# Kernel optimization log

Hardware: AMD Instinct MI355X
Metric: run time of the kernel (lower is better)

Reference implementation:

```python
import jax, jax.numpy as jnp
import numpy as np

N_NODES = 100000
N_EDGES = 500000
HEADS = 4
HID = 64
N_GRAPHS = 512
EPS_SM = 1e-8
EPS_BN = 1e-5


def setup_inputs() -> dict:
    key = jax.random.key(0)
    ks = jax.random.split(key, 8)
    x = jax.random.normal(ks[0], (N_NODES, HID), dtype=jnp.float32)
    edge_index = jax.random.randint(ks[1], (2, N_EDGES), 0, N_NODES, dtype=jnp.int64)
    batch = jnp.sort(jax.random.randint(ks[2], (N_NODES,), 0, N_GRAPHS, dtype=jnp.int64))
    Ws = jax.random.normal(ks[3], (3, HEADS * HID, HID), dtype=jnp.float32) * 0.08
    att_src = jax.random.normal(ks[4], (3, HEADS, HID), dtype=jnp.float32) * 0.1
    att_dst = jax.random.normal(ks[5], (3, HEADS, HID), dtype=jnp.float32) * 0.1
    bn_gamma = jnp.ones((2, HID), dtype=jnp.float32)
    bn_beta = jnp.zeros((2, HID), dtype=jnp.float32)
    bn_mean = jnp.zeros((2, HID), dtype=jnp.float32)
    bn_var = jnp.ones((2, HID), dtype=jnp.float32)
    fc_w = jax.random.normal(ks[6], (2, HID), dtype=jnp.float32) * 0.1
    fc_b = jnp.zeros((2,), dtype=jnp.float32)
    return {"x": x, "edge_index": edge_index, "batch": batch, "Ws": Ws,
            "att_src": att_src, "att_dst": att_dst, "bn_gamma": bn_gamma,
            "bn_beta": bn_beta, "bn_mean": bn_mean, "bn_var": bn_var,
            "fc_w": fc_w, "fc_b": fc_b}


def gat_layer(x, row, col, W, a_src, a_dst):
    # x: [N, F] -> h: [N, H, C]
    n = x.shape[0]
    h = (x @ W.T).reshape(n, HEADS, HID)
    a_s = jnp.sum(h * a_src[None], axis=-1)          # [N, H]
    a_d = jnp.sum(h * a_dst[None], axis=-1)          # [N, H]
    e = a_s[row] + a_d[col]                          # [E, H]
    e = jnp.where(e >= 0, e, 0.2 * e)                # LeakyReLU(0.2)
    # segment softmax over destination node (col)
    e_max = jax.ops.segment_max(e, col, num_segments=n)  # [N, H]
    p = jnp.exp(e - e_max[col])
    p_sum = jax.ops.segment_sum(p, col, num_segments=n)
    alpha = p / (p_sum[col] + EPS_SM)                # [E, H]
    msg = h[row] * alpha[:, :, None]                 # [E, H, C]
    out = jax.ops.segment_sum(msg, col, num_segments=n)  # [N, H, C]
    return out.mean(axis=1)                          # [N, C]


def reference(x, edge_index, batch, Ws, att_src, att_dst,
              bn_gamma, bn_beta, bn_mean, bn_var, fc_w, fc_b):
    row, col = edge_index[0], edge_index[1]
    h = x
    for i in range(2):  # first num_layers-1 layers: conv -> BN(eval) -> ReLU
        h = gat_layer(h, row, col, Ws[i], att_src[i], att_dst[i])
        h = (h - bn_mean[i]) * jax.lax.rsqrt(bn_var[i] + EPS_BN) * bn_gamma[i] + bn_beta[i]
        h = jax.nn.relu(h)
        # dropout is inactive in eval mode
    h = gat_layer(h, row, col, Ws[2], att_src[2], att_dst[2])
    # global mean pool over graphs in batch
    sums = jax.ops.segment_sum(h, batch, num_segments=N_GRAPHS)          # [G, C]
    cnts = jax.ops.segment_sum(jnp.ones_like(batch, dtype=h.dtype), batch,
                               num_segments=N_GRAPHS)                    # [G]
    pooled = sums / jnp.maximum(cnts, 1.0)[:, None]
    return pooled @ fc_w.T + fc_b                                        # [G, out]
```

## Files before the change

### kernel.cpp

```cpp
#include <hip/hip_runtime.h>


#define THREADS 256
#define LDP 36
#define SFP 68

__global__ __launch_bounds__(THREADS) void k_prep(
    const float* __restrict__ Ws, const float* __restrict__ att_src,
    const float* __restrict__ att_dst, float* __restrict__ fold)
{
    int idx = blockIdx.x * THREADS + threadIdx.x;
    if (idx >= 3 * 2 * 4 * 64) return;
    int k = idx & 63, head = (idx >> 6) & 3, sd = (idx >> 8) & 1, l = idx >> 9;
    const float* att = (sd ? att_dst : att_src) + l * 256 + head * 64;
    const float* Wb  = Ws + (size_t)l * 16384 + (size_t)head * 64 * 64;
    float s = 0.f;
    #pragma unroll
    for (int c = 0; c < 64; ++c) s = fmaf(Wb[(size_t)c * 64 + k], att[c], s);
    fold[((l * 2 + sd) * 4 + head) * 64 + k] = s;
}

__global__ __launch_bounds__(THREADS) void k_gemm(
    const float* __restrict__ x, const float* __restrict__ W,
    const float* __restrict__ fold_l,
    float* __restrict__ h, float* __restrict__ a_s, float* __restrict__ a_d, int n)
{
    __shared__ float xs[128][LDP];
    __shared__ float ws[128][LDP];
    __shared__ float sf[8 * SFP];
    const int tid  = threadIdx.x;
    const int tc   = tid & 15;
    const int tr   = tid >> 4;
    const int row0 = blockIdx.x * 128;
    const int col0 = blockIdx.y * 128;
    const bool gy0 = (blockIdx.y == 0);

    if (gy0) {
        #pragma unroll
        for (int j = 0; j < 2; ++j) {
            int idx = j * 256 + tid;
            sf[(idx >> 6) * SFP + (idx & 63)] = fold_l[idx];
        }
    }

    float acc[8][8];
    #pragma unroll
    for (int i = 0; i < 8; ++i)
        #pragma unroll
        for (int j = 0; j < 8; ++j) acc[i][j] = 0.f;
    float pa[4] = {0.f, 0.f, 0.f, 0.f};

    for (int ks2 = 0; ks2 < 2; ++ks2) {
        #pragma unroll
        for (int i = 0; i < 4; ++i) {
            int flat4 = i * 256 + tid;
            int r  = flat4 >> 3;
            int c4 = flat4 & 7;
            int gr = row0 + r;
            float4 v = make_float4(0.f, 0.f, 0.f, 0.f);
            if (gr < n) v = *(const float4*)(x + (size_t)gr * 64 + ks2 * 32 + c4 * 4);
            *(float4*)&xs[r][c4 * 4] = v;
            int gp = col0 + r;
            int pr = (gp & 3) * 64 + (gp >> 2);
            float4 wv = *(const float4*)(W + (size_t)pr * 64 + ks2 * 32 + c4 * 4);
            *(float4*)&ws[r][c4 * 4] = wv;
        }
        __syncthreads();

        #pragma unroll 1
        for (int ks = 0; ks < 8; ++ks) {
            float4 xr[8];
            #pragma unroll
            for (int i = 0; i < 8; ++i) xr[i] = *(const float4*)&xs[tr + 16 * i][ks * 4];
            #pragma unroll
            for (int j = 0; j < 8; ++j) {
                float4 w4 = *(const float4*)&ws[tc + 16 * j][ks * 4];
                #pragma unroll
                for (int i = 0; i < 8; ++i) {
                    acc[i][j] = fmaf(xr[i].x, w4.x, acc[i][j]);
                    acc[i][j] = fmaf(xr[i].y, w4.y, acc[i][j]);
                    acc[i][j] = fmaf(xr[i].z, w4.z, acc[i][j]);
                    acc[i][j] = fmaf(xr[i].w, w4.w, acc[i][j]);
                }
            }
        }
        if (gy0) {
            const int vec = tid & 7;
            #pragma unroll
            for (int j = 0; j < 4; ++j) {
                int row = j * 32 + (tid >> 3);
                float s = 0.f;
                #pragma unroll
                for (int k = 0; k < 32; ++k)
                    s = fmaf(xs[row][k], sf[vec * SFP + ks2 * 32 + k], s);
                pa[j] += s;
            }
        }
        __syncthreads();
    }

    #pragma unroll
    for (int i = 0; i < 8; ++i) {
        int r = row0 + tr + 16 * i;
        if (r < n) {
            float* hp = h + (size_t)r * 256 + col0 + tc;
            #pragma unroll
            for (int j = 0; j < 8; ++j) hp[16 * j] = acc[i][j];
        }
    }
    if (gy0) {
        const int vec = tid & 7;
        #pragma unroll
        for (int j = 0; j < 4; ++j) {
            int rr = row0 + j * 32 + (tid >> 3);
            if (rr < n) {
                if (vec < 4) a_s[(size_t)rr * 4 + vec] = pa[j];
                else         a_d[(size_t)rr * 4 + (vec - 4)] = pa[j];
            }
        }
    }
}

__global__ __launch_bounds__(THREADS) void k_hist(
    const int* __restrict__ col, int* __restrict__ hist, int E)
{
    int e = blockIdx.x * THREADS + threadIdx.x;
    if (e < E) atomicAdd(hist + col[e], 1);
}

__global__ __launch_bounds__(THREADS) void k_scan1(
    const int* __restrict__ hist, int* __restrict__ offs, int* __restrict__ partials, int n)
{
    __shared__ int buf0[256], buf1[256];
    int tid = threadIdx.x;
    int i = blockIdx.x * 256 + tid;
    int v = (i < n) ? hist[i] : 0;
    buf0[tid] = v;
    __syncthreads();
    int* src = buf0; int* dst = buf1;
    #pragma unroll
    for (int off = 1; off < 256; off <<= 1) {
        int t = src[tid];
        if (tid >= off) t += src[tid - off];
        dst[tid] = t;
        __syncthreads();
        int* tmp = src; src = dst; dst = tmp;
    }
    if (i < n) offs[i] = src[tid] - v;
    if (tid == 255) partials[blockIdx.x] = src[255];
}

__global__ __launch_bounds__(512) void k_scan2(int* __restrict__ partials, int nb)
{
    __shared__ int buf0[512], buf1[512];
    int tid = threadIdx.x;
    int v = (tid < nb) ? partials[tid] : 0;
    buf0[tid] = v;
    __syncthreads();
    int* src = buf0; int* dst = buf1;
    #pragma unroll
    for (int off = 1; off < 512; off <<= 1) {
        int t = src[tid];
        if (tid >= off) t += src[tid - off];
        dst[tid] = t;
        __syncthreads();
        int* tmp = src; src = dst; dst = tmp;
    }
    if (tid < nb) partials[tid] = src[tid] - v;
}

__global__ __launch_bounds__(THREADS) void k_scan3(
    int* __restrict__ offs, const int* __restrict__ partials, int n)
{
    int i = blockIdx.x * THREADS + threadIdx.x;
    if (i < n) offs[i] += partials[i >> 8];
}

__global__ __launch_bounds__(THREADS) void k_scatter(
    const int* __restrict__ row, const int* __restrict__ col,
    const int* __restrict__ offs, int* __restrict__ tmpc,
    int* __restrict__ rs, int* __restrict__ pose, int E)
{
    int e = blockIdx.x * THREADS + threadIdx.x;
    if (e >= E) return;
    int c = col[e];
    int pos = offs[c] + atomicAdd(tmpc + c, 1);
    rs[pos] = row[e];
    pose[e] = pos;
}

__global__ __launch_bounds__(THREADS) void k_score_ns(
    const int* __restrict__ row, const int* __restrict__ col,
    const int* __restrict__ pose,
    const float* __restrict__ a_s, const float* __restrict__ a_d,
    float* __restrict__ alpha, int E)
{
    int e = blockIdx.x * THREADS + threadIdx.x;
    if (e >= E) return;
    int r = row[e], c = col[e];
    float4 as = *(const float4*)(a_s + (size_t)r * 4);
    float4 ad = *(const float4*)(a_d + (size_t)c * 4);
    float v0 = as.x + ad.x, v1 = as.y + ad.y, v2 = as.z + ad.z, v3 = as.w + ad.w;
    v0 = v0 >= 0.f ? v0 : 0.2f * v0;
    v1 = v1 >= 0.f ? v1 : 0.2f * v1;
    v2 = v2 >= 0.f ? v2 : 0.2f * v2;
    v3 = v3 >= 0.f ? v3 : 0.2f * v3;
    *(float4*)(alpha + (size_t)pose[e] * 4) = make_float4(v0, v1, v2, v3);
}

__global__ __launch_bounds__(THREADS) void k_alpha2(
    const int* __restrict__ offs, const int* __restrict__ deg,
    float* __restrict__ alpha, float* __restrict__ psum, int n)
{
    int v = blockIdx.x * THREADS + threadIdx.x;
    if (v >= n) return;
    const int start = offs[v];
    const int d     = deg[v];
    float m0 = -1e30f, m1 = -1e30f, m2 = -1e30f, m3 = -1e30f;
    for (int i = 0; i < d; ++i) {
        float4 s = *(const float4*)(alpha + (size_t)(start + i) * 4);
        m0 = fmaxf(m0, s.x); m1 = fmaxf(m1, s.y);
        m2 = fmaxf(m2, s.z); m3 = fmaxf(m3, s.w);
    }
    float ps0 = 0.f, ps1 = 0.f, ps2 = 0.f, ps3 = 0.f;
    for (int i = 0; i < d; ++i) {
        float4 s = *(const float4*)(alpha + (size_t)(start + i) * 4);
        float p0 = __expf(s.x - m0), p1 = __expf(s.y - m1);
        float p2 = __expf(s.z - m2), p3 = __expf(s.w - m3);
        ps0 += p0; ps1 += p1; ps2 += p2; ps3 += p3;
        *(float4*)(alpha + (size_t)(start + i) * 4) = make_float4(p0, p1, p2, p3);
    }
    *(float4*)(psum + (size_t)v * 4) = make_float4(ps0, ps1, ps2, ps3);
}

__global__ __launch_bounds__(THREADS) void k_gat(
    const int* __restrict__ rs, const int* __restrict__ offs, const int* __restrict__ deg,
    const float* __restrict__ alpha, const float* __restrict__ psum,
    const float* __restrict__ h,
    const float* __restrict__ bng, const float* __restrict__ bnb,
    const float* __restrict__ bnm, const float* __restrict__ bnv, int use_bn,
    float* __restrict__ out, int n)
{
    int wid  = (blockIdx.x * THREADS + threadIdx.x) >> 6;
    int lane = threadIdx.x & 63;
    if (wid >= n) return;
    const int start = offs[wid];
    const int d     = deg[wid];
    float4 ps = *(const float4*)(psum + (size_t)wid * 4);
    const float i0 = 0.25f / (ps.x + 1e-8f), i1 = 0.25f / (ps.y + 1e-8f);
    const float i2 = 0.25f / (ps.z + 1e-8f), i3 = 0.25f / (ps.w + 1e-8f);

    float acc = 0.f;
    for (int i = 0; i < d; ++i) {
        int r = rs[start + i];
        float4 a = *(const float4*)(alpha + (size_t)(start + i) * 4);
        float4 v = *(const float4*)(h + (size_t)r * 256 + lane * 4);
        acc = fmaf(a.x * i0, v.x, acc);
        acc = fmaf(a.y * i1, v.y, acc);
        acc = fmaf(a.z * i2, v.z, acc);
        acc = fmaf(a.w * i3, v.w, acc);
    }
    if (use_bn) {
        float scale = bng[lane] * rsqrtf(bnv[lane] + 1e-5f);
        float shift = bnb[lane] - bnm[lane] * scale;
        acc = fmaxf(fmaf(acc, scale, shift), 0.f);
    }
    out[(size_t)wid * 64 + lane] = acc;
}

#define POOL_CHUNK 32
__global__ __launch_bounds__(THREADS) void k_pool(
    const float* __restrict__ xf, const int* __restrict__ batch,
    float* __restrict__ sums, float* __restrict__ cnt, int n)
{
    int wid  = (blockIdx.x * THREADS + threadIdx.x) >> 6;
    int lane = threadIdx.x & 63;
    int n0 = wid * POOL_CHUNK;
    if (n0 >= n) return;
    int n1 = min(n0 + POOL_CHUNK, n);
    int g = batch[n0];
    float acc = 0.f, c = 0.f;
    for (int i = n0; i < n1; ++i) {
        int gi = batch[i];
        if (gi != g) {
            atomicAdd(sums + (size_t)g * 64 + lane, acc);
            if (lane == 0) atomicAdd(cnt + g, c);
            g = gi; acc = 0.f; c = 0.f;
        }
        acc += xf[(size_t)i * 64 + lane];
        c += 1.f;
    }
    atomicAdd(sums + (size_t)g * 64 + lane, acc);
    if (lane == 0) atomicAdd(cnt + g, c);
}

__global__ __launch_bounds__(THREADS) void k_fc(
    const float* __restrict__ sums, const float* __restrict__ cnt,
    const float* __restrict__ fw, const float* __restrict__ fb,
    float* __restrict__ out, int G)
{
    int g = blockIdx.x * THREADS + threadIdx.x;
    if (g >= G) return;
    float cdiv = fmaxf(cnt[g], 1.f);
    float o0 = fb[0], o1 = fb[1];
    for (int k = 0; k < 64; ++k) {
        float p = sums[(size_t)g * 64 + k] / cdiv;
        o0 = fmaf(p, fw[k], o0);
        o1 = fmaf(p, fw[64 + k], o1);
    }
    out[(size_t)g * 2 + 0] = o0;
    out[(size_t)g * 2 + 1] = o1;
}

static inline size_t align256(size_t x) { return (x + 255) & ~(size_t)255; }

extern "C" void kernel_launch(void* const* d_in, const int* in_sizes, int n_in,
                              void* d_out, int out_size, void* d_ws, size_t ws_size,
                              hipStream_t stream)
{
    const float* x        = (const float*)d_in[0];
    const int*   eidx     = (const int*)d_in[1];
    const int*   batch    = (const int*)d_in[2];
    const float* Ws       = (const float*)d_in[3];
    const float* att_src  = (const float*)d_in[4];
    const float* att_dst  = (const float*)d_in[5];
    const float* bn_gamma = (const float*)d_in[6];
    const float* bn_beta  = (const float*)d_in[7];
    const float* bn_mean  = (const float*)d_in[8];
    const float* bn_var   = (const float*)d_in[9];
    const float* fc_w     = (const float*)d_in[10];
    const float* fc_b     = (const float*)d_in[11];

    const int N = in_sizes[0] / 64;
    const int E = in_sizes[1] / 2;
    const int G = 512;
    const int* row = eidx;
    const int* col = eidx + E;

    char* p = (char*)d_ws;
    float* h     = (float*)p; p += align256((size_t)N * 256 * 4);
    float* a_s   = (float*)p; p += align256((size_t)N * 4 * 4);
    float* a_d   = (float*)p; p += align256((size_t)N * 4 * 4);
    float* psum  = (float*)p; p += align256((size_t)N * 4 * 4);
    float* xb0   = (float*)p; p += align256((size_t)N * 64 * 4);
    float* xb1   = (float*)p; p += align256((size_t)N * 64 * 4);
    int*   hist  = (int*)p;   p += align256((size_t)N * 4);
    int*   offs  = (int*)p;   p += align256((size_t)N * 4);
    int*   tmpc  = (int*)p;   p += align256((size_t)N * 4);
    int*   part  = (int*)p;   p += align256((size_t)1024 * 4);
    int*   rs    = (int*)p;   p += align256((size_t)E * 4);
    int*   pose  = (int*)p;   p += align256((size_t)E * 4);
    float* alpha = (float*)p; p += align256((size_t)E * 4 * 4);
    float* fold  = (float*)p; p += align256((size_t)1536 * 4);
    float* sums  = (float*)p; p += align256((size_t)G * 64 * 4);
    float* cnt   = (float*)p; p += align256((size_t)G * 4);
    (void)ws_size; (void)n_in; (void)out_size;

    const int nb = (N + 255) / 256;
    const int eb = (E + THREADS - 1) / THREADS;

    k_prep<<<6, THREADS, 0, stream>>>(Ws, att_src, att_dst, fold);
    hipMemsetAsync(hist, 0, (size_t)N * 4, stream);
    hipMemsetAsync(tmpc, 0, (size_t)N * 4, stream);
    k_hist<<<eb, THREADS, 0, stream>>>(col, hist, E);
    k_scan1<<<nb, THREADS, 0, stream>>>(hist, offs, part, N);
    k_scan2<<<1, 512, 0, stream>>>(part, nb);
    k_scan3<<<nb, THREADS, 0, stream>>>(offs, part, N);
    k_scatter<<<eb, THREADS, 0, stream>>>(row, col, offs, tmpc, rs, pose, E);

    const float* xin = x;
    for (int l = 0; l < 3; ++l) {
        float* xout = (l == 1) ? xb1 : xb0;
        dim3 ggrid((N + 127) / 128, 2);
        k_gemm<<<ggrid, THREADS, 0, stream>>>(
            xin, Ws + (size_t)l * 16384, fold + (size_t)l * 512, h, a_s, a_d, N);
        k_score_ns<<<eb, THREADS, 0, stream>>>(row, col, pose, a_s, a_d, alpha, E);
        k_alpha2<<<nb, THREADS, 0, stream>>>(offs, hist, alpha, psum, N);
        k_gat<<<((size_t)N * 64 + THREADS - 1) / THREADS, THREADS, 0, stream>>>(
            rs, offs, hist, alpha, psum, h,
            bn_gamma + l * 64, bn_beta + l * 64, bn_mean + l * 64, bn_var + l * 64,
            (l < 2) ? 1 : 0, xout, N);
        xin = xout;
    }

    hipMemsetAsync(sums, 0, (size_t)G * 64 * 4, stream);
    hipMemsetAsync(cnt, 0, (size_t)G * 4, stream);
    int pool_waves = (N + POOL_CHUNK - 1) / POOL_CHUNK;
    k_pool<<<((size_t)pool_waves * 64 + THREADS - 1) / THREADS, THREADS, 0, stream>>>(
        xin, batch, sums, cnt, N);
    k_fc<<<(G + THREADS - 1) / THREADS, THREADS, 0, stream>>>(
        sums, cnt, fc_w, fc_b, (float*)d_out, G);
}
```

Measured before the change: 594.7 us.

## Drop softmax max-subtraction and fuse normalization into aggregation kernel

Computes exp of the LeakyReLU score directly in the edge scoring kernel, without subtracting the per-destination max. The per-node sum is then accumulated inside the aggregation kernel alongside the weighted message sum. This removes the separate per-node softmax kernel, its two passes over alpha and the psum buffer, saving one launch and memory traffic per layer. The risk is overflow or precision loss without max subtraction, and the small epsilon now acts on an unshifted sum, so results change slightly.

```diff
diff --git a/kernel.cpp b/kernel.cpp
--- a/kernel.cpp
+++ b/kernel.cpp
@@ -189,7 +189,7 @@
     pose[e] = pos;
 }
 
-__global__ __launch_bounds__(THREADS) void k_score_ns(
+__global__ __launch_bounds__(THREADS) void k_score_exp(
     const int* __restrict__ row, const int* __restrict__ col,
     const int* __restrict__ pose,
     const float* __restrict__ a_s, const float* __restrict__ a_d,
@@ -205,38 +205,13 @@
     v1 = v1 >= 0.f ? v1 : 0.2f * v1;
     v2 = v2 >= 0.f ? v2 : 0.2f * v2;
     v3 = v3 >= 0.f ? v3 : 0.2f * v3;
-    *(float4*)(alpha + (size_t)pose[e] * 4) = make_float4(v0, v1, v2, v3);
-}
-
-__global__ __launch_bounds__(THREADS) void k_alpha2(
-    const int* __restrict__ offs, const int* __restrict__ deg,
-    float* __restrict__ alpha, float* __restrict__ psum, int n)
-{
-    int v = blockIdx.x * THREADS + threadIdx.x;
-    if (v >= n) return;
-    const int start = offs[v];
-    const int d     = deg[v];
-    float m0 = -1e30f, m1 = -1e30f, m2 = -1e30f, m3 = -1e30f;
-    for (int i = 0; i < d; ++i) {
-        float4 s = *(const float4*)(alpha + (size_t)(start + i) * 4);
-        m0 = fmaxf(m0, s.x); m1 = fmaxf(m1, s.y);
-        m2 = fmaxf(m2, s.z); m3 = fmaxf(m3, s.w);
-    }
-    float ps0 = 0.f, ps1 = 0.f, ps2 = 0.f, ps3 = 0.f;
-    for (int i = 0; i < d; ++i) {
-        float4 s = *(const float4*)(alpha + (size_t)(start + i) * 4);
-        float p0 = __expf(s.x - m0), p1 = __expf(s.y - m1);
-        float p2 = __expf(s.z - m2), p3 = __expf(s.w - m3);
-        ps0 += p0; ps1 += p1; ps2 += p2; ps3 += p3;
-        *(float4*)(alpha + (size_t)(start + i) * 4) = make_float4(p0, p1, p2, p3);
-    }
-    *(float4*)(psum + (size_t)v * 4) = make_float4(ps0, ps1, ps2, ps3);
+    *(float4*)(alpha + (size_t)pose[e] * 4) =
+        make_float4(__expf(v0), __expf(v1), __expf(v2), __expf(v3));
 }
 
 __global__ __launch_bounds__(THREADS) void k_gat(
     const int* __restrict__ rs, const int* __restrict__ offs, const int* __restrict__ deg,
-    const float* __restrict__ alpha, const float* __restrict__ psum,
-    const float* __restrict__ h,
+    const float* __restrict__ alpha, const float* __restrict__ h,
     const float* __restrict__ bng, const float* __restrict__ bnb,
     const float* __restrict__ bnm, const float* __restrict__ bnv, int use_bn,
     float* __restrict__ out, int n)
@@ -246,20 +221,21 @@
     if (wid >= n) return;
     const int start = offs[wid];
     const int d     = deg[wid];
-    float4 ps = *(const float4*)(psum + (size_t)wid * 4);
-    const float i0 = 0.25f / (ps.x + 1e-8f), i1 = 0.25f / (ps.y + 1e-8f);
-    const float i2 = 0.25f / (ps.z + 1e-8f), i3 = 0.25f / (ps.w + 1e-8f);
-
-    float acc = 0.f;
+
+    float acc0 = 0.f, acc1 = 0.f, acc2 = 0.f, acc3 = 0.f;
+    float ps0 = 0.f, ps1 = 0.f, ps2 = 0.f, ps3 = 0.f;
     for (int i = 0; i < d; ++i) {
         int r = rs[start + i];
         float4 a = *(const float4*)(alpha + (size_t)(start + i) * 4);
         float4 v = *(const float4*)(h + (size_t)r * 256 + lane * 4);
-        acc = fmaf(a.x * i0, v.x, acc);
-        acc = fmaf(a.y * i1, v.y, acc);
-        acc = fmaf(a.z * i2, v.z, acc);
-        acc = fmaf(a.w * i3, v.w, acc);
-    }
+        ps0 += a.x; ps1 += a.y; ps2 += a.z; ps3 += a.w;
+        acc0 = fmaf(a.x, v.x, acc0);
+        acc1 = fmaf(a.y, v.y, acc1);
+        acc2 = fmaf(a.z, v.z, acc2);
+        acc3 = fmaf(a.w, v.w, acc3);
+    }
+    float acc = acc0 * (0.25f / (ps0 + 1e-8f)) + acc1 * (0.25f / (ps1 + 1e-8f))
+              + acc2 * (0.25f / (ps2 + 1e-8f)) + acc3 * (0.25f / (ps3 + 1e-8f));
     if (use_bn) {
         float scale = bng[lane] * rsqrtf(bnv[lane] + 1e-5f);
         float shift = bnb[lane] - bnm[lane] * scale;
@@ -341,7 +317,6 @@
     float* h     = (float*)p; p += align256((size_t)N * 256 * 4);
     float* a_s   = (float*)p; p += align256((size_t)N * 4 * 4);
     float* a_d   = (float*)p; p += align256((size_t)N * 4 * 4);
-    float* psum  = (float*)p; p += align256((size_t)N * 4 * 4);
     float* xb0   = (float*)p; p += align256((size_t)N * 64 * 4);
     float* xb1   = (float*)p; p += align256((size_t)N * 64 * 4);
     int*   hist  = (int*)p;   p += align256((size_t)N * 4);
@@ -374,10 +349,9 @@
         dim3 ggrid((N + 127) / 128, 2);
         k_gemm<<<ggrid, THREADS, 0, stream>>>(
             xin, Ws + (size_t)l * 16384, fold + (size_t)l * 512, h, a_s, a_d, N);
-        k_score_ns<<<eb, THREADS, 0, stream>>>(row, col, pose, a_s, a_d, alpha, E);
-        k_alpha2<<<nb, THREADS, 0, stream>>>(offs, hist, alpha, psum, N);
+        k_score_exp<<<eb, THREADS, 0, stream>>>(row, col, pose, a_s, a_d, alpha, E);
         k_gat<<<((size_t)N * 64 + THREADS - 1) / THREADS, THREADS, 0, stream>>>(
-            rs, offs, hist, alpha, psum, h,
+            rs, offs, hist, alpha, h,
             bn_gamma + l * 64, bn_beta + l * 64, bn_mean + l * 64, bn_var + l * 64,
             (l < 2) ? 1 : 0, xout, N);
         xin = xout;
```

New measurement: 566.2 us. 1.05x faster.
